# Performance work log

Hardware: AMD Instinct MI355X
Metric: run time of the kernel (lower is better)

The kernel has to match this reference:

```python
import jax, jax.numpy as jnp
import numpy as np

B, T, D = 2, 2048, 2048
H, HKV, HD = 32, 8, 64
THETA = 3.0
EPS = 1e-6
SCALE = HD ** -0.5


def _rms(x, w):
    # x: [..., HD]
    return x * jax.lax.rsqrt(jnp.mean(x * x, axis=-1, keepdims=True) + EPS) * w


def _rope(x):
    # x: [B, h, T, HD]; interleaved-pair rotation, matching RotaryEmbedding
    hd = x.shape[-1]
    inv_freq = 1.0 / (THETA ** (jnp.arange(0, hd, 2, dtype=jnp.float32) / hd))  # [hd/2]
    t = jnp.arange(x.shape[-2], dtype=jnp.float32)
    f = t[:, None] * inv_freq[None, :]  # [T, hd/2]
    c, s = jnp.cos(f), jnp.sin(f)
    x1, x2 = x[..., 0::2], x[..., 1::2]
    return jnp.stack([x1 * c - x2 * s, x1 * s + x2 * c], axis=-1).reshape(x.shape)


def setup_inputs() -> dict:
    key = jax.random.key(0)
    ks = jax.random.split(key, 6)
    x = jax.random.normal(ks[0], (B, T, D), dtype=jnp.float32)
    w_scale = 1.0 / np.sqrt(D)
    Wq = jax.random.normal(ks[1], (H * HD, D), dtype=jnp.float32) * w_scale
    Wk = jax.random.normal(ks[2], (HKV * HD, D), dtype=jnp.float32) * w_scale
    Wv = jax.random.normal(ks[3], (HKV * HD, D), dtype=jnp.float32) * w_scale
    Wo = jax.random.normal(ks[4], (D, H * HD), dtype=jnp.float32) * (1.0 / np.sqrt(H * HD))
    q_norm_w = jnp.ones((HD,), dtype=jnp.float32)
    k_norm_w = jnp.ones((HD,), dtype=jnp.float32)
    causal = jnp.tril(jnp.ones((T, T), dtype=bool))
    mask = jnp.where(causal, 0.0, -1e9).astype(jnp.float32)[None, None]  # [1,1,T,T]
    return dict(x=x, Wq=Wq, Wk=Wk, Wv=Wv, Wo=Wo, q_norm_w=q_norm_w, k_norm_w=k_norm_w, mask=mask)


def reference(x, Wq, Wk, Wv, Wo, q_norm_w, k_norm_w, mask):
    b, t, _ = x.shape
    q = (x @ Wq.T).reshape(b, t, H, HD).transpose(0, 2, 1, 3)      # [B,H,T,HD]
    k = (x @ Wk.T).reshape(b, t, HKV, HD).transpose(0, 2, 1, 3)    # [B,HKV,T,HD]
    v = (x @ Wv.T).reshape(b, t, HKV, HD).transpose(0, 2, 1, 3)
    q = _rms(q, q_norm_w)
    k = _rms(k, k_norm_w)
    q = _rope(q)
    k = _rope(k)
    rep = H // HKV
    k = jnp.repeat(k, rep, axis=1)  # GQA expansion -> [B,H,T,HD]
    v = jnp.repeat(v, rep, axis=1)
    scores = jnp.einsum('bhqd,bhkd->bhqk', q, k) * SCALE + mask
    attn = jax.nn.softmax(scores, axis=-1)
    out = jnp.einsum('bhqk,bhkd->bhqd', attn, v)
    out = out.transpose(0, 2, 1, 3).reshape(b, t, H * HD)
    return out @ Wo.T
```

## Files before the change

### kernel.cpp

```cpp
#include <hip/hip_runtime.h>
#include <hip/hip_bf16.h>
#include <stdint.h>

#define B_ 2
#define T_ 2048
#define D_ 2048
#define H_ 32
#define HKV_ 8
#define HD_ 64
#define SCALE_ 0.125f

typedef float floatx4 __attribute__((ext_vector_type(4)));
typedef __bf16 bf16x8 __attribute__((ext_vector_type(8)));

__device__ inline floatx4 mfma16(bf16x8 a, bf16x8 b, floatx4 c) {
  return __builtin_amdgcn_mfma_f32_16x16x32_bf16(a, b, c, 0, 0, 0);
}

__device__ inline uint16_t f2bf(float f) {
  union { float f; uint32_t u; } x; x.f = f;
  uint32_t r = x.u + 0x7fffu + ((x.u >> 16) & 1u);
  return (uint16_t)(r >> 16);
}

__device__ inline uint32_t f2bf_pk(float a, float b) {
#if __has_builtin(__builtin_amdgcn_cvt_pk_bf16_f32)
  auto pk = __builtin_amdgcn_cvt_pk_bf16_f32(a, b);
  return __builtin_bit_cast(uint32_t, pk);
#else
  return (uint32_t)f2bf(a) | ((uint32_t)f2bf(b) << 16);
#endif
}

__device__ inline float fast_exp2(float x) {
#if __has_builtin(__builtin_amdgcn_exp2f)
  return __builtin_amdgcn_exp2f(x);
#else
  return __expf(x * 0.69314718056f);
#endif
}

#if __has_builtin(__builtin_amdgcn_global_load_lds)
#define HAVE_ASYNC_LDS 1
typedef const __attribute__((address_space(1))) uint32_t* gas1_u32;
typedef __attribute__((address_space(3))) uint32_t* las3_u32;
__device__ inline void g2lds16(const uint16_t* g, uint16_t* l) {
  __builtin_amdgcn_global_load_lds((gas1_u32)(const void*)g, (las3_u32)(void*)l, 16, 0, 0);
}
#endif

__global__ __launch_bounds__(256) void cvt_all(
    const float* __restrict__ x, const float* __restrict__ wq,
    const float* __restrict__ wk, const float* __restrict__ wv,
    const float* __restrict__ wo,
    uint16_t* __restrict__ xb, uint16_t* __restrict__ wqb,
    uint16_t* __restrict__ wkb, uint16_t* __restrict__ wvb,
    uint16_t* __restrict__ wob) {
  int i = blockIdx.x * 256 + threadIdx.x;
  const float* src; uint16_t* dst; int off;
  if (i < 2097152)      { src = x;  dst = xb;  off = i; }
  else if (i < 3145728) { src = wq; dst = wqb; off = i - 2097152; }
  else if (i < 3407872) { src = wk; dst = wkb; off = i - 3145728; }
  else if (i < 3670016) { src = wv; dst = wvb; off = i - 3407872; }
  else                  { src = wo; dst = wob; off = i - 3670016; }
  float4 v = ((const float4*)src)[off];
  uint64_t packed = (uint64_t)f2bf_pk(v.x, v.y) | ((uint64_t)f2bf_pk(v.z, v.w) << 32);
  ((uint64_t*)dst)[off] = packed;
}

#define BM 128
#define BN 128
#define BK 64

__device__ inline void stage64(const uint16_t* gbase, uint16_t* lds,
                               int k0, int wave, int lane) {
#ifdef HAVE_ASYNC_LDS
  #pragma unroll
  for (int c = 0; c < 4; c++) {
    int chunk = wave * 4 + c;
    int row = chunk * 8 + (lane >> 3);
    int cg  = (lane & 7) ^ ((lane >> 3) & 7);
    g2lds16(gbase + (size_t)row * D_ + k0 + cg * 8, lds + chunk * 512 + lane * 8);
  }
#else
  #pragma unroll
  for (int c = 0; c < 4; c++) {
    int chunk = wave * 4 + c;
    int row = chunk * 8 + (lane >> 3);
    int cg  = (lane & 7) ^ ((lane >> 3) & 7);
    *(uint4*)&lds[chunk * 512 + lane * 8] =
        *(const uint4*)(gbase + (size_t)row * D_ + k0 + cg * 8);
  }
#endif
}

__device__ inline bf16x8 frag64(const uint16_t* lds, int row, int cg) {
  int pcg = cg ^ (row & 7);
  return *(const bf16x8*)&lds[row * 64 + pcg * 8];
}

#define GEMM_KLOOP(Abase, Bbase)                                          \
  for (int k0 = 0; k0 < D_; k0 += BK) {                                   \
    __syncthreads();                                                      \
    stage64(Abase, As, k0, wave, lane);                                   \
    stage64(Bbase, Bs, k0, wave, lane);                                   \
    __syncthreads();                                                      \
    bf16x8 af[4][2], bfr[4][2];                                           \
    _Pragma("unroll")                                                     \
    for (int i = 0; i < 4; i++) {                                         \
      af[i][0] = frag64(As, wm + i * 16 + r16, quad);                     \
      af[i][1] = frag64(As, wm + i * 16 + r16, 4 + quad);                 \
    }                                                                     \
    _Pragma("unroll")                                                     \
    for (int j = 0; j < 4; j++) {                                         \
      bfr[j][0] = frag64(Bs, wn + j * 16 + r16, quad);                    \
      bfr[j][1] = frag64(Bs, wn + j * 16 + r16, 4 + quad);                \
    }                                                                     \
    _Pragma("unroll")                                                     \
    for (int i = 0; i < 4; i++)                                           \
      _Pragma("unroll")                                                   \
      for (int j = 0; j < 4; j++) {                                       \
        acc[i][j] = mfma16(af[i][0], bfr[j][0], acc[i][j]);               \
        acc[i][j] = mfma16(af[i][1], bfr[j][1], acc[i][j]);               \
      }                                                                   \
  }

__global__ __launch_bounds__(256) void qkv_gemm(
    const uint16_t* __restrict__ Xb, const uint16_t* __restrict__ Wqb,
    const uint16_t* __restrict__ Wkb, const uint16_t* __restrict__ Wvb,
    const float* __restrict__ qnw, const float* __restrict__ knw,
    uint16_t* __restrict__ qbf, uint16_t* __restrict__ kbf,
    uint16_t* __restrict__ vt) {
  __shared__ __align__(16) uint16_t As[BM * BK];
  __shared__ __align__(16) uint16_t Bs[BN * BK];
  const int tid = threadIdx.x;
  const int m0 = blockIdx.y * BM;
  const int n0 = blockIdx.x * BN;

  const uint16_t* Wsrc; int nbase;
  if (n0 < 2048)      { Wsrc = Wqb; nbase = 0; }
  else if (n0 < 2560) { Wsrc = Wkb; nbase = 2048; }
  else                { Wsrc = Wvb; nbase = 2560; }

  const int lane = tid & 63, wave = tid >> 6;
  const int wm = (wave >> 1) * 64, wn = (wave & 1) * 64;
  const int quad = lane >> 4, r16 = lane & 15;
  const uint16_t* Abase = Xb + (size_t)m0 * D_;
  const uint16_t* Bbase = Wsrc + (size_t)(n0 - nbase) * D_;

  floatx4 acc[4][4];
  #pragma unroll
  for (int i = 0; i < 4; i++)
    #pragma unroll
    for (int j = 0; j < 4; j++) acc[i][j] = (floatx4){0.f, 0.f, 0.f, 0.f};

  GEMM_KLOOP(Abase, Bbase)

  if (n0 < 2560) {
    const int isK = (n0 >= 2048);
    const float* nw = isK ? knw : qnw;
    const int head = (n0 - (isK ? 2048 : 0) + wn) >> 6;
    uint16_t* dst = isK ? kbf : qbf;
    const int NH = isK ? HKV_ : H_;
    float wreg[4];
    #pragma unroll
    for (int j = 0; j < 4; j++) wreg[j] = nw[j * 16 + r16];
    float freq[4];
    #pragma unroll
    for (int j = 0; j < 4; j++)
      freq[j] = exp2f((float)(j * 8 + (r16 >> 1)) * -0.0495300781f);
    #pragma unroll
    for (int i = 0; i < 4; i++) {
      #pragma unroll
      for (int r = 0; r < 4; r++) {
        float ss = 0.f;
        #pragma unroll
        for (int j = 0; j < 4; j++) ss += acc[i][j][r] * acc[i][j][r];
        #pragma unroll
        for (int off = 8; off; off >>= 1) ss += __shfl_xor(ss, off);
        float inv = rsqrtf(ss * (1.0f / HD_) + 1e-6f);
        int m = m0 + wm + i * 16 + quad * 4 + r;
        int b = m >> 11, t = m & (T_ - 1);
        size_t rowbase = (((size_t)b * NH + head) * T_ + t) * HD_;
        #pragma unroll
        for (int j = 0; j < 4; j++) {
          float vn = acc[i][j][r] * inv * wreg[j];
          float other = __shfl_xor(vn, 1);
          float f = (float)t * freq[j];
          float s, c;
          __sincosf(f, &s, &c);
          float outv = (r16 & 1) ? (other * s + vn * c) : (vn * c - other * s);
          dst[rowbase + j * 16 + r16] = f2bf(outv);
        }
      }
    }
  } else {
    #pragma unroll
    for (int i = 0; i < 4; i++)
      #pragma unroll
      for (int j = 0; j < 4; j++)
        #pragma unroll
        for (int r = 0; r < 4; r++) {
          int m = m0 + wm + i * 16 + quad * 4 + r;
          int n = n0 + wn + j * 16 + r16 - 2560;
          int b = m >> 11, t = m & (T_ - 1);
          int head = n >> 6, d = n & 63;
          vt[(((size_t)b * HKV_ + head) * HD_ + d) * T_ + t] = f2bf(acc[i][j][r]);
        }
  }
}

__global__ __launch_bounds__(256) void oproj_gemm(
    const uint16_t* __restrict__ Ab, const uint16_t* __restrict__ Bb,
    float* __restrict__ C) {
  __shared__ __align__(16) uint16_t As[BM * BK];
  __shared__ __align__(16) uint16_t Bs[BN * BK];
  const int tid = threadIdx.x;
  const int m0 = blockIdx.y * BM;
  const int n0 = blockIdx.x * BN;
  const int lane = tid & 63, wave = tid >> 6;
  const int wm = (wave >> 1) * 64, wn = (wave & 1) * 64;
  const int quad = lane >> 4, r16 = lane & 15;
  const uint16_t* Abase = Ab + (size_t)m0 * D_;
  const uint16_t* Bbase = Bb + (size_t)n0 * D_;

  floatx4 acc[4][4];
  #pragma unroll
  for (int i = 0; i < 4; i++)
    #pragma unroll
    for (int j = 0; j < 4; j++) acc[i][j] = (floatx4){0.f, 0.f, 0.f, 0.f};

  GEMM_KLOOP(Abase, Bbase)

  #pragma unroll
  for (int i = 0; i < 4; i++)
    #pragma unroll
    for (int j = 0; j < 4; j++)
      #pragma unroll
      for (int r = 0; r < 4; r++) {
        int m = m0 + wm + i * 16 + quad * 4 + r;
        int n = n0 + wn + j * 16 + r16;
        C[(size_t)m * D_ + n] = acc[i][j][r];
      }
}

#define AT_PAD 68
#define LOG2E 1.44269504089f

__global__ __launch_bounds__(256) void attn(const uint16_t* __restrict__ qb,
                                            const uint16_t* __restrict__ kb,
                                            const uint16_t* __restrict__ vtb,
                                            uint16_t* __restrict__ ao) {
  const int tid = threadIdx.x;
  const int wave = tid >> 6, lane = tid & 63;
  const int quad = lane >> 4, r16 = lane & 15;
  const int h = blockIdx.y, b = blockIdx.z;
  const int kvh = h >> 2;

  const uint16_t* Q  = qb  + ((size_t)b * H_ + h) * T_ * HD_;
  const uint16_t* K  = kb  + ((size_t)b * HKV_ + kvh) * T_ * HD_;
  const uint16_t* Vt = vtb + ((size_t)b * HKV_ + kvh) * (size_t)HD_ * T_;

  __shared__ __align__(16) uint16_t Kl[64 * AT_PAD];
  __shared__ __align__(16) uint16_t Vl[64 * AT_PAD];
  __shared__ __align__(16) uint16_t Pl[4][32 * AT_PAD];
  uint16_t* myP = Pl[wave];

  const int srow = tid >> 2, sseg = tid & 3;

  for (int pass = 0; pass < 2; pass++) {
    const int qt = pass ? (int)blockIdx.x : 15 - (int)blockIdx.x;
    const int q0 = qt * 128;
    const int Rw = q0 + wave * 32;

    bf16x8 aq[2][2];
    #pragma unroll
    for (int m = 0; m < 2; m++)
      #pragma unroll
      for (int hh = 0; hh < 2; hh++)
        aq[m][hh] = *(const bf16x8*)(Q + (size_t)(Rw + m * 16 + r16) * HD_ + hh * 32 + quad * 8);

    floatx4 o[2][4];
    float l[2][4];
    #pragma unroll
    for (int m = 0; m < 2; m++) {
      #pragma unroll
      for (int j = 0; j < 4; j++) o[m][j] = (floatx4){0.f, 0.f, 0.f, 0.f};
      #pragma unroll
      for (int r = 0; r < 4; r++) l[m][r] = 0.f;
    }

    const int wkend = Rw + 31;
    const int iters = 2 * qt + 2;

    for (int it = 0; it < iters; it++) {
      const int kt = it * 64;
      {
        const uint16_t* kg = K + (size_t)(kt + srow) * HD_ + sseg * 16;
        uint4 k0 = *(const uint4*)kg;
        uint4 k1 = *(const uint4*)(kg + 8);
        const uint16_t* vg = Vt + (size_t)srow * T_ + kt + sseg * 16;
        uint4 v0 = *(const uint4*)vg;
        uint4 v1 = *(const uint4*)(vg + 8);
        __syncthreads();
        *(uint4*)&Kl[srow * AT_PAD + sseg * 16] = k0;
        *(uint4*)&Kl[srow * AT_PAD + sseg * 16 + 8] = k1;
        *(uint4*)&Vl[srow * AT_PAD + sseg * 16] = v0;
        *(uint4*)&Vl[srow * AT_PAD + sseg * 16 + 8] = v1;
        __syncthreads();
      }
      if (kt > wkend) continue;

      const bool need_mask = (kt + 63) > Rw;

      floatx4 s[2][4];
      #pragma unroll
      for (int m = 0; m < 2; m++)
        #pragma unroll
        for (int nc = 0; nc < 4; nc++) s[m][nc] = (floatx4){0.f, 0.f, 0.f, 0.f};
      #pragma unroll
      for (int nc = 0; nc < 4; nc++) {
        bf16x8 kf0 = *(const bf16x8*)&Kl[(nc * 16 + r16) * AT_PAD + quad * 8];
        bf16x8 kf1 = *(const bf16x8*)&Kl[(nc * 16 + r16) * AT_PAD + 32 + quad * 8];
        #pragma unroll
        for (int m = 0; m < 2; m++) {
          s[m][nc] = mfma16(aq[m][0], kf0, s[m][nc]);
          s[m][nc] = mfma16(aq[m][1], kf1, s[m][nc]);
        }
      }

      #pragma unroll
      for (int m = 0; m < 2; m++) {
        #pragma unroll
        for (int nc = 0; nc < 4; nc++) {
          float pv[4];
          #pragma unroll
          for (int r = 0; r < 4; r++) {
            pv[r] = fast_exp2(fmaf(s[m][nc][r], SCALE_ * LOG2E, -8.0f * LOG2E));
            if (need_mask) {
              int col = kt + nc * 16 + r16;
              int rowq = Rw + m * 16 + quad * 4 + r;
              if (col > rowq) pv[r] = 0.f;
            }
            l[m][r] += pv[r];
          }
          int base = m * 16 + quad * 4;
          int cc = nc * 16 + r16;
          uint32_t u01 = f2bf_pk(pv[0], pv[1]);
          uint32_t u23 = f2bf_pk(pv[2], pv[3]);
          myP[(base + 0) * AT_PAD + cc] = (uint16_t)u01;
          myP[(base + 1) * AT_PAD + cc] = (uint16_t)(u01 >> 16);
          myP[(base + 2) * AT_PAD + cc] = (uint16_t)u23;
          myP[(base + 3) * AT_PAD + cc] = (uint16_t)(u23 >> 16);
        }
      }
      __asm__ __volatile__("s_waitcnt lgkmcnt(0)" ::: "memory");

      bf16x8 ap[2][2];
      #pragma unroll
      for (int m = 0; m < 2; m++) {
        ap[m][0] = *(const bf16x8*)&myP[(m * 16 + r16) * AT_PAD + quad * 8];
        ap[m][1] = *(const bf16x8*)&myP[(m * 16 + r16) * AT_PAD + 32 + quad * 8];
      }
      #pragma unroll
      for (int jn = 0; jn < 4; jn++) {
        bf16x8 vf0 = *(const bf16x8*)&Vl[(jn * 16 + r16) * AT_PAD + quad * 8];
        bf16x8 vf1 = *(const bf16x8*)&Vl[(jn * 16 + r16) * AT_PAD + 32 + quad * 8];
        #pragma unroll
        for (int m = 0; m < 2; m++) {
          o[m][jn] = mfma16(ap[m][0], vf0, o[m][jn]);
          o[m][jn] = mfma16(ap[m][1], vf1, o[m][jn]);
        }
      }
    }

    #pragma unroll
    for (int m = 0; m < 2; m++)
      #pragma unroll
      for (int r = 0; r < 4; r++) {
        #pragma unroll
        for (int off = 8; off; off >>= 1) l[m][r] += __shfl_xor(l[m][r], off);
      }
    #pragma unroll
    for (int m = 0; m < 2; m++)
      #pragma unroll
      for (int jn = 0; jn < 4; jn++) {
        float inv0 = 1.0f / l[m][0], inv1 = 1.0f / l[m][1];
        float inv2 = 1.0f / l[m][2], inv3 = 1.0f / l[m][3];
        uint32_t u01 = f2bf_pk(o[m][jn][0] * inv0, o[m][jn][1] * inv1);
        uint32_t u23 = f2bf_pk(o[m][jn][2] * inv2, o[m][jn][3] * inv3);
        int t0 = Rw + m * 16 + quad * 4;
        size_t base = ((size_t)b * T_ + t0) * (H_ * HD_) + h * HD_ + jn * 16 + r16;
        ao[base]                = (uint16_t)u01;
        ao[base + 1 * H_ * HD_] = (uint16_t)(u01 >> 16);
        ao[base + 2 * H_ * HD_] = (uint16_t)u23;
        ao[base + 3 * H_ * HD_] = (uint16_t)(u23 >> 16);
      }
  }
}

extern "C" void kernel_launch(void* const* d_in, const int* in_sizes, int n_in,
                              void* d_out, int out_size, void* d_ws, size_t ws_size,
                              hipStream_t stream) {
  const float* x  = (const float*)d_in[0];
  const float* Wq = (const float*)d_in[1];
  const float* Wk = (const float*)d_in[2];
  const float* Wv = (const float*)d_in[3];
  const float* Wo = (const float*)d_in[4];
  const float* qw = (const float*)d_in[5];
  const float* kw = (const float*)d_in[6];
  float* out = (float*)d_out;

  char* ws = (char*)d_ws;
  uint16_t* xb  = (uint16_t*)(ws);
  uint16_t* wqb = (uint16_t*)(ws + 16777216);
  uint16_t* wkb = (uint16_t*)(ws + 25165824);
  uint16_t* wvb = (uint16_t*)(ws + 27262976);
  uint16_t* wob = (uint16_t*)(ws + 29360128);
  uint16_t* qbf = (uint16_t*)(ws + 37748736);
  uint16_t* kbf = (uint16_t*)(ws + 54525952);
  uint16_t* vtb = (uint16_t*)(ws + 58720256);
  uint16_t* aob = xb;

  cvt_all<<<18432, 256, 0, stream>>>(x, Wq, Wk, Wv, Wo, xb, wqb, wkb, wvb, wob);

  qkv_gemm<<<dim3(24, 32), 256, 0, stream>>>(xb, wqb, wkb, wvb, qw, kw, qbf, kbf, vtb);

  attn<<<dim3(8, 32, 2), 256, 0, stream>>>(qbf, kbf, vtb, aob);

  oproj_gemm<<<dim3(16, 32), 256, 0, stream>>>(aob, wob, out);
}
```

Baseline: 357.6 us.

## Restructure attention to compute S transposed and feed P to PV MFMA from registers

The attention kernel now computes S^T = K·Q^T with 16x16x32 MFMA. The resulting accumulator layout is used directly as the A operand of a 16x16x16 bf16 MFMA for P·V, so the per-wave P scratch in LDS and its round trip go away. Query tiles shrink to 64 rows (16 per wave) with twice as many blocks, and causal skipping is done per 16-key sub-tile. K/V LDS tiles use an XOR swizzle instead of padding, with an optional async global-to-LDS path. The risks are smaller per-wave tiles that reduce K/V reuse, and more MFMA instructions of the smaller K size.

```diff
diff --git a/kernel.cpp b/kernel.cpp
--- a/kernel.cpp
+++ b/kernel.cpp
@@ -12,9 +12,20 @@
 
 typedef float floatx4 __attribute__((ext_vector_type(4)));
 typedef __bf16 bf16x8 __attribute__((ext_vector_type(8)));
+typedef __bf16 bf16x4 __attribute__((ext_vector_type(4)));
+typedef short short4v __attribute__((ext_vector_type(4)));
 
 __device__ inline floatx4 mfma16(bf16x8 a, bf16x8 b, floatx4 c) {
   return __builtin_amdgcn_mfma_f32_16x16x32_bf16(a, b, c, 0, 0, 0);
+}
+
+__device__ inline floatx4 mfma16k16(bf16x4 a, bf16x4 b, floatx4 c) {
+#if __has_builtin(__builtin_amdgcn_mfma_f32_16x16x16_bf16)
+  return __builtin_amdgcn_mfma_f32_16x16x16_bf16(a, b, c, 0, 0, 0);
+#else
+  return __builtin_amdgcn_mfma_f32_16x16x16bf16_1k(
+      __builtin_bit_cast(short4v, a), __builtin_bit_cast(short4v, b), c, 0, 0, 0);
+#endif
 }
 
 __device__ inline uint16_t f2bf(float f) {
@@ -244,7 +255,6 @@
       }
 }
 
-#define AT_PAD 68
 #define LOG2E 1.44269504089f
 
 __global__ __launch_bounds__(256) void attn(const uint16_t* __restrict__ qb,
@@ -261,141 +271,98 @@
   const uint16_t* K  = kb  + ((size_t)b * HKV_ + kvh) * T_ * HD_;
   const uint16_t* Vt = vtb + ((size_t)b * HKV_ + kvh) * (size_t)HD_ * T_;
 
-  __shared__ __align__(16) uint16_t Kl[64 * AT_PAD];
-  __shared__ __align__(16) uint16_t Vl[64 * AT_PAD];
-  __shared__ __align__(16) uint16_t Pl[4][32 * AT_PAD];
-  uint16_t* myP = Pl[wave];
-
-  const int srow = tid >> 2, sseg = tid & 3;
+  __shared__ __align__(16) uint16_t Kl[64 * 64];
+  __shared__ __align__(16) uint16_t Vl[64 * 64];
 
   for (int pass = 0; pass < 2; pass++) {
-    const int qt = pass ? (int)blockIdx.x : 15 - (int)blockIdx.x;
-    const int q0 = qt * 128;
-    const int Rw = q0 + wave * 32;
-
-    bf16x8 aq[2][2];
-    #pragma unroll
-    for (int m = 0; m < 2; m++)
-      #pragma unroll
-      for (int hh = 0; hh < 2; hh++)
-        aq[m][hh] = *(const bf16x8*)(Q + (size_t)(Rw + m * 16 + r16) * HD_ + hh * 32 + quad * 8);
-
-    floatx4 o[2][4];
-    float l[2][4];
-    #pragma unroll
-    for (int m = 0; m < 2; m++) {
-      #pragma unroll
-      for (int j = 0; j < 4; j++) o[m][j] = (floatx4){0.f, 0.f, 0.f, 0.f};
-      #pragma unroll
-      for (int r = 0; r < 4; r++) l[m][r] = 0.f;
-    }
-
-    const int wkend = Rw + 31;
-    const int iters = 2 * qt + 2;
-
+    const int qt = pass ? (int)blockIdx.x : 31 - (int)blockIdx.x;
+    const int q0 = qt * 64;
+    const int Rw = q0 + wave * 16;
+
+    bf16x8 bq[2];
+    #pragma unroll
+    for (int hh = 0; hh < 2; hh++)
+      bq[hh] = *(const bf16x8*)(Q + (size_t)(Rw + r16) * HD_ + hh * 32 + quad * 8);
+
+    floatx4 o[4];
+    float l = 0.f;
+    #pragma unroll
+    for (int jn = 0; jn < 4; jn++) o[jn] = (floatx4){0.f, 0.f, 0.f, 0.f};
+
+    const int iters = qt + 1;
     for (int it = 0; it < iters; it++) {
       const int kt = it * 64;
-      {
-        const uint16_t* kg = K + (size_t)(kt + srow) * HD_ + sseg * 16;
-        uint4 k0 = *(const uint4*)kg;
-        uint4 k1 = *(const uint4*)(kg + 8);
-        const uint16_t* vg = Vt + (size_t)srow * T_ + kt + sseg * 16;
-        uint4 v0 = *(const uint4*)vg;
-        uint4 v1 = *(const uint4*)(vg + 8);
-        __syncthreads();
-        *(uint4*)&Kl[srow * AT_PAD + sseg * 16] = k0;
-        *(uint4*)&Kl[srow * AT_PAD + sseg * 16 + 8] = k1;
-        *(uint4*)&Vl[srow * AT_PAD + sseg * 16] = v0;
-        *(uint4*)&Vl[srow * AT_PAD + sseg * 16 + 8] = v1;
-        __syncthreads();
-      }
-      if (kt > wkend) continue;
-
-      const bool need_mask = (kt + 63) > Rw;
-
-      floatx4 s[2][4];
-      #pragma unroll
-      for (int m = 0; m < 2; m++)
-        #pragma unroll
-        for (int nc = 0; nc < 4; nc++) s[m][nc] = (floatx4){0.f, 0.f, 0.f, 0.f};
-      #pragma unroll
-      for (int nc = 0; nc < 4; nc++) {
-        bf16x8 kf0 = *(const bf16x8*)&Kl[(nc * 16 + r16) * AT_PAD + quad * 8];
-        bf16x8 kf1 = *(const bf16x8*)&Kl[(nc * 16 + r16) * AT_PAD + 32 + quad * 8];
-        #pragma unroll
-        for (int m = 0; m < 2; m++) {
-          s[m][nc] = mfma16(aq[m][0], kf0, s[m][nc]);
-          s[m][nc] = mfma16(aq[m][1], kf1, s[m][nc]);
+      __syncthreads();
+#ifdef HAVE_ASYNC_LDS
+      #pragma unroll
+      for (int c = 0; c < 2; c++) {
+        int row = wave * 16 + c * 8 + (lane >> 3);
+        int cg  = (lane & 7) ^ ((lane >> 3) & 7);
+        g2lds16(K  + (size_t)(kt + row) * HD_ + cg * 8, Kl + (wave * 16 + c * 8) * 64 + lane * 8);
+        g2lds16(Vt + (size_t)row * T_ + kt + cg * 8,    Vl + (wave * 16 + c * 8) * 64 + lane * 8);
+      }
+#else
+      #pragma unroll
+      for (int c = 0; c < 2; c++) {
+        int row = wave * 16 + c * 8 + (lane >> 3);
+        int cg  = (lane & 7) ^ ((lane >> 3) & 7);
+        *(uint4*)&Kl[(wave * 16 + c * 8) * 64 + lane * 8] =
+            *(const uint4*)(K + (size_t)(kt + row) * HD_ + cg * 8);
+        *(uint4*)&Vl[(wave * 16 + c * 8) * 64 + lane * 8] =
+            *(const uint4*)(Vt + (size_t)row * T_ + kt + cg * 8);
+      }
+#endif
+      __syncthreads();
+
+      #pragma unroll
+      for (int mt = 0; mt < 4; mt++) {
+        if (kt + mt * 16 > Rw + 15) continue;
+        bf16x8 kf0 = frag64(Kl, mt * 16 + r16, quad);
+        bf16x8 kf1 = frag64(Kl, mt * 16 + r16, 4 + quad);
+        floatx4 st = (floatx4){0.f, 0.f, 0.f, 0.f};
+        st = mfma16(kf0, bq[0], st);
+        st = mfma16(kf1, bq[1], st);
+        const bool needm = (kt + mt * 16 + 15) > Rw;
+        float pv[4];
+        #pragma unroll
+        for (int r = 0; r < 4; r++) {
+          pv[r] = fast_exp2(fmaf(st[r], SCALE_ * LOG2E, -8.0f * LOG2E));
+          if (needm) {
+            int kcol = kt + mt * 16 + quad * 4 + r;
+            if (kcol > Rw + r16) pv[r] = 0.f;
+          }
+          l += pv[r];
         }
-      }
-
-      #pragma unroll
-      for (int m = 0; m < 2; m++) {
-        #pragma unroll
-        for (int nc = 0; nc < 4; nc++) {
-          float pv[4];
-          #pragma unroll
-          for (int r = 0; r < 4; r++) {
-            pv[r] = fast_exp2(fmaf(s[m][nc][r], SCALE_ * LOG2E, -8.0f * LOG2E));
-            if (need_mask) {
-              int col = kt + nc * 16 + r16;
-              int rowq = Rw + m * 16 + quad * 4 + r;
-              if (col > rowq) pv[r] = 0.f;
-            }
-            l[m][r] += pv[r];
-          }
-          int base = m * 16 + quad * 4;
-          int cc = nc * 16 + r16;
-          uint32_t u01 = f2bf_pk(pv[0], pv[1]);
-          uint32_t u23 = f2bf_pk(pv[2], pv[3]);
-          myP[(base + 0) * AT_PAD + cc] = (uint16_t)u01;
-          myP[(base + 1) * AT_PAD + cc] = (uint16_t)(u01 >> 16);
-          myP[(base + 2) * AT_PAD + cc] = (uint16_t)u23;
-          myP[(base + 3) * AT_PAD + cc] = (uint16_t)(u23 >> 16);
+        uint64_t pu = (uint64_t)f2bf_pk(pv[0], pv[1]) |
+                      ((uint64_t)f2bf_pk(pv[2], pv[3]) << 32);
+        bf16x4 pa = __builtin_bit_cast(bf16x4, pu);
+        #pragma unroll
+        for (int jn = 0; jn < 4; jn++) {
+          int vrow = jn * 16 + r16;
+          int pcg = (mt * 2 + (quad >> 1)) ^ (vrow & 7);
+          bf16x4 vf = *(const bf16x4*)&Vl[vrow * 64 + pcg * 8 + (quad & 1) * 4];
+          o[jn] = mfma16k16(pa, vf, o[jn]);
         }
       }
-      __asm__ __volatile__("s_waitcnt lgkmcnt(0)" ::: "memory");
-
-      bf16x8 ap[2][2];
-      #pragma unroll
-      for (int m = 0; m < 2; m++) {
-        ap[m][0] = *(const bf16x8*)&myP[(m * 16 + r16) * AT_PAD + quad * 8];
-        ap[m][1] = *(const bf16x8*)&myP[(m * 16 + r16) * AT_PAD + 32 + quad * 8];
-      }
-      #pragma unroll
-      for (int jn = 0; jn < 4; jn++) {
-        bf16x8 vf0 = *(const bf16x8*)&Vl[(jn * 16 + r16) * AT_PAD + quad * 8];
-        bf16x8 vf1 = *(const bf16x8*)&Vl[(jn * 16 + r16) * AT_PAD + 32 + quad * 8];
-        #pragma unroll
-        for (int m = 0; m < 2; m++) {
-          o[m][jn] = mfma16(ap[m][0], vf0, o[m][jn]);
-          o[m][jn] = mfma16(ap[m][1], vf1, o[m][jn]);
-        }
-      }
     }
 
-    #pragma unroll
-    for (int m = 0; m < 2; m++)
-      #pragma unroll
-      for (int r = 0; r < 4; r++) {
-        #pragma unroll
-        for (int off = 8; off; off >>= 1) l[m][r] += __shfl_xor(l[m][r], off);
-      }
-    #pragma unroll
-    for (int m = 0; m < 2; m++)
-      #pragma unroll
-      for (int jn = 0; jn < 4; jn++) {
-        float inv0 = 1.0f / l[m][0], inv1 = 1.0f / l[m][1];
-        float inv2 = 1.0f / l[m][2], inv3 = 1.0f / l[m][3];
-        uint32_t u01 = f2bf_pk(o[m][jn][0] * inv0, o[m][jn][1] * inv1);
-        uint32_t u23 = f2bf_pk(o[m][jn][2] * inv2, o[m][jn][3] * inv3);
-        int t0 = Rw + m * 16 + quad * 4;
-        size_t base = ((size_t)b * T_ + t0) * (H_ * HD_) + h * HD_ + jn * 16 + r16;
-        ao[base]                = (uint16_t)u01;
-        ao[base + 1 * H_ * HD_] = (uint16_t)(u01 >> 16);
-        ao[base + 2 * H_ * HD_] = (uint16_t)u23;
-        ao[base + 3 * H_ * HD_] = (uint16_t)(u23 >> 16);
-      }
+    l += __shfl_xor(l, 16);
+    l += __shfl_xor(l, 32);
+    float lq[4];
+    #pragma unroll
+    for (int r = 0; r < 4; r++) lq[r] = __shfl(l, quad * 4 + r);
+
+    #pragma unroll
+    for (int jn = 0; jn < 4; jn++) {
+      uint32_t u01 = f2bf_pk(o[jn][0] / lq[0], o[jn][1] / lq[1]);
+      uint32_t u23 = f2bf_pk(o[jn][2] / lq[2], o[jn][3] / lq[3]);
+      int t0 = Rw + quad * 4;
+      size_t base = ((size_t)b * T_ + t0) * (H_ * HD_) + h * HD_ + jn * 16 + r16;
+      ao[base]                = (uint16_t)u01;
+      ao[base + 1 * H_ * HD_] = (uint16_t)(u01 >> 16);
+      ao[base + 2 * H_ * HD_] = (uint16_t)u23;
+      ao[base + 3 * H_ * HD_] = (uint16_t)(u23 >> 16);
+    }
   }
 }
 
@@ -426,7 +393,7 @@
 
   qkv_gemm<<<dim3(24, 32), 256, 0, stream>>>(xb, wqb, wkb, wvb, qw, kw, qbf, kbf, vtb);
 
-  attn<<<dim3(8, 32, 2), 256, 0, stream>>>(qbf, kbf, vtb, aob);
+  attn<<<dim3(16, 32, 2), 256, 0, stream>>>(qbf, kbf, vtb, aob);
 
   oproj_gemm<<<dim3(16, 32), 256, 0, stream>>>(aob, wob, out);
 }
```

Result: faster. 339.7 us (-5.0%).
